# Kernel optimization log

Measured on AMD Instinct MI355X. Metric: run time of the kernel, lower is better.

Reference implementation:

```python
import jax, jax.numpy as jnp
import numpy as np

B, N, T, H = 32, 512, 3, 8
F_IN, F_HID, F_OUT = 768, 64, 64
NEG_SLOPE = 0.2
NEG_INF = -1e9


def setup_inputs() -> dict:
    key = jax.random.key(0)
    ks = jax.random.split(key, 16)
    s = 0.05
    emb = jax.random.normal(ks[0], (B, N, F_IN), jnp.float32)
    adj = jax.random.randint(ks[1], (B, N, N), 0, 2).astype(jnp.int32)
    adj = adj.at[:, jnp.arange(N), jnp.arange(N)].set(1)  # self loops so no empty rows
    vt_idx = jax.random.randint(ks[2], (B, N), 0, T)
    v_types = jax.nn.one_hot(vt_idx, T, dtype=jnp.float32)
    # layer 1 GAT params: per-type weights [T,H,f_in,f_out]
    w1 = jax.random.normal(ks[3], (T, H, F_IN, F_HID), jnp.float32) * s
    a_src1 = jax.random.normal(ks[4], (H, F_HID), jnp.float32) * s
    a_dst1 = jax.random.normal(ks[5], (H, F_HID), jnp.float32) * s
    b1 = jnp.zeros((F_HID,), jnp.float32)
    # layer 2 GAT (single head, f_in = H*F_HID)
    w2 = jax.random.normal(ks[6], (T, 1, H * F_HID, F_OUT), jnp.float32) * s
    a_src2 = jax.random.normal(ks[7], (1, F_OUT), jnp.float32) * s
    a_dst2 = jax.random.normal(ks[8], (1, F_OUT), jnp.float32) * s
    b2 = jnp.zeros((F_OUT,), jnp.float32)
    # MLP classifier: fc1 d->3d, fc2 3d->d, fc3 d->2
    fc1_w = jax.random.normal(ks[9], (F_OUT, 3 * F_OUT), jnp.float32) * s
    fc1_b = jnp.zeros((3 * F_OUT,), jnp.float32)
    fc2_w = jax.random.normal(ks[10], (3 * F_OUT, F_OUT), jnp.float32) * s
    fc2_b = jnp.zeros((F_OUT,), jnp.float32)
    fc3_w = jax.random.normal(ks[11], (F_OUT, 2), jnp.float32) * s
    fc3_b = jnp.zeros((2,), jnp.float32)
    return dict(emb=emb, adj=adj, v_types=v_types,
                w1=w1, a_src1=a_src1, a_dst1=a_dst1, b1=b1,
                w2=w2, a_src2=a_src2, a_dst2=a_dst2, b2=b2,
                fc1_w=fc1_w, fc1_b=fc1_b, fc2_w=fc2_w, fc2_b=fc2_b,
                fc3_w=fc3_w, fc3_b=fc3_b)


def _leaky_relu(x):
    return jnp.where(x >= 0, x, NEG_SLOPE * x)


def _gat(h, adj_mask, vt, w, a_src, a_dst, bias):
    # h: [B,N,f_in], vt: [B,N,T] one-hot, w: [T,Hd,f_in,f_out]
    # per-type projection then select node's type
    hpt = jnp.einsum('bni,thio->bntho', h, w)          # [B,N,T,Hd,f_out]
    hp = jnp.einsum('bnt,bntho->bnho', vt, hpt)        # [B,N,Hd,f_out]
    src = jnp.einsum('bnho,ho->bhn', hp, a_src)        # [B,Hd,N]
    dst = jnp.einsum('bnho,ho->bhn', hp, a_dst)
    e = _leaky_relu(src[:, :, :, None] + dst[:, :, None, :])  # [B,Hd,N,N]
    e = jnp.where(adj_mask[:, None, :, :], e, NEG_INF)
    attn = jax.nn.softmax(e, axis=-1)                  # attn_dropout=0.0 -> identity
    out = jnp.einsum('bhnm,bmho->bhno', attn, hp) + bias
    return out                                         # [B,Hd,N,f_out]


def reference(emb, adj, v_types, w1, a_src1, a_dst1, b1,
              w2, a_src2, a_dst2, b2,
              fc1_w, fc1_b, fc2_w, fc2_b, fc3_w, fc3_b):
    adj_mask = adj > 0
    x = _gat(emb, adj_mask, v_types, w1, a_src1, a_dst1, b1)    # [B,H,N,F_HID]
    x = jnp.transpose(x, (0, 2, 1, 3)).reshape(B, N, H * F_HID)  # concat heads
    x = jax.nn.elu(x)                                            # dropout: eval mode (identity)
    x = _gat(x, adj_mask, v_types, w2, a_src2, a_dst2, b2)       # [B,1,N,F_OUT]
    x = jax.nn.elu(x)
    x = x[:, 0, :, :]                                            # squeeze head dim -> [B,N,F_OUT]
    left = x[:, 0, :]
    right = x[:, 1, :]
    v = left * right
    v = jax.nn.relu(v @ fc1_w + fc1_b)
    v = jax.nn.relu(v @ fc2_w + fc2_b)
    scores = v @ fc3_w + fc3_b
    return jax.nn.log_softmax(scores, axis=1)
```

## Files before the change

kernel.cpp:

```cpp
#include <hip/hip_runtime.h>

#define BB   32
#define NN   512
#define NH   8
#define FIN  768
#define FHID 64
#define NROWS (BB*NN)

typedef __attribute__((ext_vector_type(8))) short bf16x8;
typedef __attribute__((ext_vector_type(4))) short s16x4;
typedef __attribute__((ext_vector_type(4))) float f32x4;
typedef unsigned long long u64;
typedef unsigned short u16;

__device__ __forceinline__ float lrelu_f(float s){ return fmaxf(s, 0.2f*s); }
__device__ __forceinline__ float elu_f(float s){ return s > 0.f ? s : expm1f(s); }
__device__ __forceinline__ short f2bf(float f){
  unsigned u = __float_as_uint(f);
  return (short)((u + 0x7fffu + ((u >> 16) & 1u)) >> 16);
}
__device__ __forceinline__ float bf2f(short s){
  return __uint_as_float(((unsigned)(u16)s) << 16);
}
__device__ __forceinline__ unsigned cvt_pk_bf16(float lo, float hi){
  unsigned r;
  asm("v_cvt_pk_bf16_f32 %0, %1, %2" : "=v"(r) : "v"(lo), "v"(hi));
  return r;
}

__global__ __launch_bounds__(256) void prep_kernel(
    const int* __restrict__ adj,
    u64* __restrict__ maskw)
{
  int row  = blockIdx.x * 4 + (threadIdx.x >> 6);
  int lane = threadIdx.x & 63;
  const int* arow = adj + (long)row * NN;
  #pragma unroll
  for (int w = 0; w < 8; ++w) {
    u64 bal = __ballot(arow[w*64 + lane] > 0);
    if (lane == 0) maskw[(long)row*8 + w] = bal;
  }
}

__global__ __launch_bounds__(256) void rowlist_kernel(
    const float* __restrict__ vt,
    int* __restrict__ rowlist, int* __restrict__ counts)
{
  __shared__ int lc[3];
  __shared__ int lbase[3];
  int tid = threadIdx.x;
  int row = blockIdx.x * 256 + tid;
  if (tid < 3) lc[tid] = 0;
  __syncthreads();
  const float* v = vt + (long)row*3;
  int t = v[1] > 0.5f ? 1 : (v[2] > 0.5f ? 2 : 0);
  int p = atomicAdd(&lc[t], 1);
  __syncthreads();
  if (tid < 3) lbase[tid] = atomicAdd(&counts[tid], lc[tid]);
  __syncthreads();
  rowlist[t*NROWS + lbase[t] + p] = row;
}

__global__ __launch_bounds__(256) void conv_w(
    const float* __restrict__ w1, const float* __restrict__ w2,
    u16* __restrict__ w1t, u16* __restrict__ w2t)
{
  __shared__ float tile[64][68];
  int bid = blockIdx.x, tid = threadIdx.x;
  const float* src; u16* dst; int K;
  if (bid < 24) { src = w1 + (long)bid*768*64; dst = w1t + (long)bid*64*768; K = 768; }
  else { int t = bid - 24; src = w2 + (long)t*512*64; dst = w2t + (long)t*64*512; K = 512; }
  int kq = blockIdx.y;
  int kstart = kq * (K >> 2), kend = kstart + (K >> 2);

  for (int k0 = kstart; k0 < kend; k0 += 64) {
    __syncthreads();
    #pragma unroll
    for (int i = 0; i < 4; ++i) {
      int kk = i*16 + (tid >> 4);
      int oo = (tid & 15) * 4;
      float4 v = *(const float4*)(src + (long)(k0 + kk)*64 + oo);
      *(float4*)&tile[kk][oo] = v;
    }
    __syncthreads();
    int o = tid >> 2, kp = (tid & 3) * 16;
    bf16x8 r0, r1;
    #pragma unroll
    for (int j = 0; j < 8; ++j) r0[j] = f2bf(tile[kp + j][o]);
    #pragma unroll
    for (int j = 0; j < 8; ++j) r1[j] = f2bf(tile[kp + 8 + j][o]);
    u16* d = dst + (long)o*K + k0 + kp;
    *(bf16x8*)d = r0;
    *(bf16x8*)(d + 8) = r1;
  }
}

__global__ __launch_bounds__(256) void gemm1_mfma(
    const float* __restrict__ emb,
    const u16* __restrict__ w1t,
    const int* __restrict__ rowlist, const int* __restrict__ counts,
    u16* __restrict__ hp1b)
{
  int i   = blockIdx.x;
  int t   = i / 352;
  int r   = i - t*352;
  int cnt = counts[t];
  int xcd = r & 7;
  int q   = r >> 3;
  int hb  = q & 3;
  int rb  = (q >> 2) * 8 + xcd;
  int r0  = rb * 64;
  if (r0 >= cnt) return;

  __shared__ short aT[2][4*66*8];
  __shared__ short bT[2][4*130*8];
  __shared__ int rowsS[64];

  int tid = threadIdx.x;
  if (tid < 64) {
    int rr = r0 + tid;
    rowsS[tid] = (rr < cnt) ? rowlist[t*NROWS + rr] : -1;
  }
  __syncthreads();

  int ar = tid >> 2, ac = tid & 3;
  int sg = rowsS[ar]; if (sg < 0) sg = rowsS[0];
  const float* aP = emb + (long)sg*768;

  int colb = tid >> 2, off = tid & 3;
  const u16* bP1 = w1t + (((long)t*8 + hb*2 + 0)*64 + colb)*768;
  const u16* bP2 = w1t + (((long)t*8 + hb*2 + 1)*64 + colb)*768;

  int wv = tid >> 6, l = tid & 63;
  int wr = wv >> 1, wc = wv & 1;
  int l15 = l & 15, lg = l >> 4;

  int aw0 = (( (ac>>1)     )*66 + ar)*8 + (ac&1)*4;
  int aw1 = (( 2 + (ac>>1) )*66 + ar)*8 + (ac&1)*4;
  int bw0 = (off*130 + colb     )*8;
  int bw1 = (off*130 + colb + 64)*8;

  f32x4 acc[2][4];
  #pragma unroll
  for (int fr = 0; fr < 2; ++fr)
    #pragma unroll
    for (int cf = 0; cf < 4; ++cf) acc[fr][cf] = (f32x4){0.f,0.f,0.f,0.f};

  float4 ra0 = *(const float4*)(aP + ac*4);
  float4 ra1 = *(const float4*)(aP + 16 + ac*4);
  bf16x8 rb1 = *(const bf16x8*)(bP1 + off*8);
  bf16x8 rb2 = *(const bf16x8*)(bP2 + off*8);
  {
    s16x4 w0, w1;
    w0[0]=f2bf(ra0.x); w0[1]=f2bf(ra0.y); w0[2]=f2bf(ra0.z); w0[3]=f2bf(ra0.w);
    w1[0]=f2bf(ra1.x); w1[1]=f2bf(ra1.y); w1[2]=f2bf(ra1.z); w1[3]=f2bf(ra1.w);
    *(s16x4*)&aT[0][aw0] = w0;
    *(s16x4*)&aT[0][aw1] = w1;
    *(bf16x8*)&bT[0][bw0] = rb1;
    *(bf16x8*)&bT[0][bw1] = rb2;
  }
  __syncthreads();

  int cur = 0;
  for (int k0 = 0; k0 < 768; k0 += 32) {
    bool more = (k0 + 32 < 768);
    if (more) {
      ra0 = *(const float4*)(aP + k0 + 32 + ac*4);
      ra1 = *(const float4*)(aP + k0 + 48 + ac*4);
      rb1 = *(const bf16x8*)(bP1 + k0 + 32 + off*8);
      rb2 = *(const bf16x8*)(bP2 + k0 + 32 + off*8);
    }
    bf16x8 af[2], bfr[4];
    #pragma unroll
    for (int fr = 0; fr < 2; ++fr)
      af[fr] = *(const bf16x8*)&aT[cur][(lg*66 + wr*32 + fr*16 + l15)*8];
    #pragma unroll
    for (int cf = 0; cf < 4; ++cf)
      bfr[cf] = *(const bf16x8*)&bT[cur][(lg*130 + wc*64 + cf*16 + l15)*8];
    #pragma unroll
    for (int fr = 0; fr < 2; ++fr)
      #pragma unroll
      for (int cf = 0; cf < 4; ++cf)
        acc[fr][cf] = __builtin_amdgcn_mfma_f32_16x16x32_bf16(af[fr], bfr[cf], acc[fr][cf], 0, 0, 0);
    if (more) {
      s16x4 w0, w1;
      w0[0]=f2bf(ra0.x); w0[1]=f2bf(ra0.y); w0[2]=f2bf(ra0.z); w0[3]=f2bf(ra0.w);
      w1[0]=f2bf(ra1.x); w1[1]=f2bf(ra1.y); w1[2]=f2bf(ra1.z); w1[3]=f2bf(ra1.w);
      *(s16x4*)&aT[cur^1][aw0] = w0;
      *(s16x4*)&aT[cur^1][aw1] = w1;
      *(bf16x8*)&bT[cur^1][bw0] = rb1;
      *(bf16x8*)&bT[cur^1][bw1] = rb2;
    }
    __syncthreads();
    cur ^= 1;
  }

  #pragma unroll
  for (int fr = 0; fr < 2; ++fr) {
    #pragma unroll
    for (int r4 = 0; r4 < 4; ++r4) {
      int rloc = wr*32 + fr*16 + lg*4 + r4;
      int rg = rowsS[rloc];
      if (rg < 0) continue;
      long obase = ((long)(rg >> 9) * 8) * 32768 + (long)(rg & 511) * 64;
      #pragma unroll
      for (int cf = 0; cf < 4; ++cf) {
        int c = wc*64 + cf*16 + l15;
        hp1b[obase + (long)(hb*2 + (c >> 6))*32768 + (c & 63)] = (u16)f2bf(acc[fr][cf][r4]);
      }
    }
  }
}

__global__ __launch_bounds__(256) void gemm2_mfma(
    const u16* __restrict__ xbf,
    const u16* __restrict__ w2t,
    const int* __restrict__ rowlist, const int* __restrict__ counts,
    float* __restrict__ hp2)
{
  int i   = blockIdx.x;
  int t   = i >> 8;
  int cnt = counts[t];
  int r0  = (i & 255) * 64;
  if (r0 >= cnt) return;

  __shared__ short aT[4*66*8];
  __shared__ short bT[4*66*8];
  __shared__ int rowsS[64];

  int tid = threadIdx.x;
  if (tid < 64) {
    int rr = r0 + tid;
    rowsS[tid] = (rr < cnt) ? rowlist[t*NROWS + rr] : -1;
  }
  __syncthreads();

  int ar = tid >> 2, ac = tid & 3;
  int sg = rowsS[ar]; if (sg < 0) sg = rowsS[0];
  long apart = ((long)(sg >> 9) * 8) * 32768 + (long)(sg & 511) * 64;

  int colb = tid >> 2, off = tid & 3;
  const u16* bP = w2t + ((long)t*64 + colb)*512;

  int wv = tid >> 6, l = tid & 63;
  int l15 = l & 15, lg = l >> 4;

  f32x4 acc[4];
  #pragma unroll
  for (int cf = 0; cf < 4; ++cf) acc[cf] = (f32x4){0.f,0.f,0.f,0.f};

  int ka0 = ac*8;
  bf16x8 ra = *(const bf16x8*)(xbf + apart + (long)(ka0 >> 6)*32768 + (ka0 & 63));
  bf16x8 rb = *(const bf16x8*)(bP + off*8);

  for (int k0 = 0; k0 < 512; k0 += 32) {
    __syncthreads();
    *(bf16x8*)&aT[(ac*66 + ar)*8]   = ra;
    *(bf16x8*)&bT[(off*66 + colb)*8] = rb;
    __syncthreads();
    if (k0 + 32 < 512) {
      int kn = k0 + 32 + ac*8;
      ra = *(const bf16x8*)(xbf + apart + (long)(kn >> 6)*32768 + (kn & 63));
      rb = *(const bf16x8*)(bP + k0 + 32 + off*8);
    }
    bf16x8 af, bfr[4];
    af = *(const bf16x8*)&aT[(lg*66 + wv*16 + l15)*8];
    #pragma unroll
    for (int cf = 0; cf < 4; ++cf)
      bfr[cf] = *(const bf16x8*)&bT[(lg*66 + cf*16 + l15)*8];
    #pragma unroll
    for (int cf = 0; cf < 4; ++cf)
      acc[cf] = __builtin_amdgcn_mfma_f32_16x16x32_bf16(af, bfr[cf], acc[cf], 0, 0, 0);
  }

  #pragma unroll
  for (int r4 = 0; r4 < 4; ++r4) {
    int rloc = wv*16 + lg*4 + r4;
    int rg = rowsS[rloc];
    if (rg < 0) continue;
    #pragma unroll
    for (int cf = 0; cf < 4; ++cf)
      hp2[(long)rg*64 + cf*16 + l15] = acc[cf][r4];
  }
}

__global__ __launch_bounds__(1024) void gat1_attn(
    u16* __restrict__ hp1b, const u64* __restrict__ maskw,
    const float* __restrict__ a_src, const float* __restrict__ a_dst,
    const float* __restrict__ b1)
{
  extern __shared__ char smc[];
  short* hpTf = (short*)smc;
  short* pSf  = (short*)(smc + 67584);
  float* srcS = (float*)(smc + 135168);
  float* dstS = (float*)(smc + 137216);
  float* asS  = (float*)(smc + 139264);
  float* adS  = (float*)(smc + 139520);
  float* rcpS = (float*)(smc + 139776);

  int bh = blockIdx.x;
  int b = bh >> 3, h = bh & 7;
  int tid = threadIdx.x;

  if (tid < 64) asS[tid] = a_src[h*64 + tid];
  else if (tid < 128) adS[tid - 64] = a_dst[h*64 + (tid - 64)];
  __syncthreads();

  {
    int m = tid >> 1, half = tid & 1;
    int koct = m >> 3, sub = m & 7;
    const u16* hpRow = hp1b + ((long)bh*NN + m)*64 + half*32;
    float ps = 0.f, pd = 0.f;
    #pragma unroll
    for (int qq = 0; qq < 4; ++qq) {
      bf16x8 hv = *(const bf16x8*)(hpRow + qq*8);
      int o0 = half*32 + qq*8;
      #pragma unroll
      for (int j = 0; j < 8; ++j) {
        float f = bf2f(hv[j]);
        ps += f * asS[o0 + j];
        pd += f * adS[o0 + j];
        hpTf[(koct*66 + o0 + j)*8 + sub] = hv[j];
      }
    }
    ps += __shfl_xor(ps, 1);
    pd += __shfl_xor(pd, 1);
    if ((tid & 1) == 0) { srcS[m] = ps; dstS[m] = pd; }
  }
  __syncthreads();

  int wv = tid >> 6, lane = tid & 63;
  int l15 = lane & 15, lg = lane >> 4;
  int cgl = wv >> 2, nt = wv & 3;
  int o_out = nt*16 + l15;
  float bb  = b1[o_out];

  float2 dst2[4];
  #pragma unroll
  for (int jj = 0; jj < 4; ++jj)
    dst2[jj] = *(const float2*)&dstS[jj*128 + 2*lane];
  int wsel = lane >> 5;
  unsigned sh = (unsigned)((2*lane) & 63);
  int pbase = ((lane >> 2)*66)*8 + 2*(lane & 3);

  for (int sup = 0; sup < 8; ++sup) {
    #pragma unroll
    for (int rr = 0; rr < 4; ++rr) {
      int rloc = wv*4 + rr;
      int row  = sup*64 + rloc;
      float srcv = srcS[row];
      const u64* mrow = maskw + ((long)(b*NN + row))*8;
      float lsum = 0.f;
      #pragma unroll
      for (int jj = 0; jj < 4; ++jj) {
        u64 w = mrow[jj*2 + wsel];
        unsigned bits = (unsigned)(w >> sh) & 3u;
        float s0 = srcv + dst2[jj].x;
        float s1 = srcv + dst2[jj].y;
        float p0 = (bits & 1u) ? __expf(lrelu_f(s0)) : 0.f;
        float p1 = (bits & 2u) ? __expf(lrelu_f(s1)) : 0.f;
        lsum += p0 + p1;
        unsigned pk = cvt_pk_bf16(p0, p1);
        *(unsigned*)&pSf[(jj*16*66)*8 + pbase + rloc*8] = pk;
      }
      #pragma unroll
      for (int mk = 1; mk <= 32; mk <<= 1) lsum += __shfl_xor(lsum, mk);
      if (lane == 0) rcpS[rloc] = 1.f / lsum;
    }
    __syncthreads();

    f32x4 acc = {0.f, 0.f, 0.f, 0.f};
    #pragma unroll
    for (int ks = 0; ks < 16; ++ks) {
      int koct = ks*4 + lg;
      bf16x8 af = *(const bf16x8*)&pSf [(koct*66 + cgl*16 + l15)*8];
      bf16x8 bf = *(const bf16x8*)&hpTf[(koct*66 + nt*16  + l15)*8];
      acc = __builtin_amdgcn_mfma_f32_16x16x32_bf16(af, bf, acc, 0, 0, 0);
    }
    #pragma unroll
    for (int reg = 0; reg < 4; ++reg) {
      int rloc = cgl*16 + lg*4 + reg;
      int row  = sup*64 + rloc;
      float v = elu_f(acc[reg] * rcpS[rloc] + bb);
      hp1b[((long)bh*NN + row)*64 + o_out] = (u16)f2bf(v);
    }
    __syncthreads();
  }
}

__global__ __launch_bounds__(256) void gat2_final(
    const float* __restrict__ hp2, const u64* __restrict__ maskw,
    const float* __restrict__ a_src2, const float* __restrict__ a_dst2,
    const float* __restrict__ b2,
    const float* __restrict__ fc1_w, const float* __restrict__ fc1_b,
    const float* __restrict__ fc2_w, const float* __restrict__ fc2_b,
    const float* __restrict__ fc3_w, const float* __restrict__ fc3_b,
    float* __restrict__ out)
{
  extern __shared__ float sm[];
  float* hpS  = sm;
  float* dstS = hpS + 32768;
  float* srcS = dstS + 512;
  float* pS   = srcS + 512;
  float* redS = pS + 512;
  float* outS = redS + 256;
  float* vS   = outS + 128;
  float* y1S  = vS + 64;
  float* redM = y1S + 192;
  float4* hpS4 = (float4*)hpS;

  int b = blockIdx.x;
  int tid = threadIdx.x;
  int og = tid & 15, m16 = tid >> 4;

  for (int it = 0; it < 32; ++it) {
    int fi = it*256 + tid;
    int m = fi >> 4, o4 = fi & 15;
    hpS4[m*16 + o4] = *(const float4*)(hp2 + (long)(b*NN + m)*64 + o4*4);
  }
  __syncthreads();

  float4 as4 = *(const float4*)(a_src2 + og*4);
  float4 ad4 = *(const float4*)(a_dst2 + og*4);
  for (int it = 0; it < 32; ++it) {
    int m = it*16 + m16;
    float4 hv = hpS4[m*16 + og];
    float ls = hv.x*as4.x + hv.y*as4.y + hv.z*as4.z + hv.w*as4.w;
    float ld = hv.x*ad4.x + hv.y*ad4.y + hv.z*ad4.z + hv.w*ad4.w;
    #pragma unroll
    for (int mk = 1; mk <= 8; mk <<= 1) {
      ls += __shfl_xor(ls, mk);
      ld += __shfl_xor(ld, mk);
    }
    if (og == 0) { srcS[m] = ls; dstS[m] = ld; }
  }
  __syncthreads();

  for (int n = 0; n < 2; ++n) {
    float srcv = srcS[n];
    const u64* mrow = maskw + (long)(b*NN + n)*8;
    int m0 = tid, m1 = tid + 256;
    u64 w0 = mrow[m0 >> 6], w1 = mrow[m1 >> 6];
    float s0 = srcv + dstS[m0], s1 = srcv + dstS[m1];
    float e0 = ((w0 >> (m0 & 63)) & 1ull) ? lrelu_f(s0) : -1.0e9f;
    float e1 = ((w1 >> (m1 & 63)) & 1ull) ? lrelu_f(s1) : -1.0e9f;
    float emax = fmaxf(e0, e1);
    #pragma unroll
    for (int mk = 1; mk <= 32; mk <<= 1) emax = fmaxf(emax, __shfl_xor(emax, mk));
    if ((tid & 63) == 0) redM[tid >> 6] = emax;
    __syncthreads();
    emax = fmaxf(fmaxf(redM[0], redM[1]), fmaxf(redM[2], redM[3]));
    float p0 = __expf(e0 - emax), p1 = __expf(e1 - emax);
    pS[m0] = p0; pS[m1] = p1;
    float lsum = p0 + p1;
    #pragma unroll
    for (int mk = 1; mk <= 32; mk <<= 1) lsum += __shfl_xor(lsum, mk);
    if ((tid & 63) == 0) redM[4 + (tid >> 6)] = lsum;
    __syncthreads();
    float rcp = 1.f / (redM[4] + redM[5] + redM[6] + redM[7]);

    float4 acc = make_float4(0.f,0.f,0.f,0.f);
    for (int mm = 0; mm < 32; ++mm) {
      int m = mm*16 + m16;
      float4 hv = hpS4[m*16 + og];
      float p = pS[m];
      acc.x += hv.x*p; acc.y += hv.y*p; acc.z += hv.z*p; acc.w += hv.w*p;
    }
    acc.x += __shfl_xor(acc.x, 16); acc.y += __shfl_xor(acc.y, 16);
    acc.z += __shfl_xor(acc.z, 16); acc.w += __shfl_xor(acc.w, 16);
    acc.x += __shfl_xor(acc.x, 32); acc.y += __shfl_xor(acc.y, 32);
    acc.z += __shfl_xor(acc.z, 32); acc.w += __shfl_xor(acc.w, 32);
    __syncthreads();
    if ((tid & 63) < 16) ((float4*)redS)[(tid >> 6)*16 + (tid & 15)] = acc;
    __syncthreads();
    if (tid < 16) {
      float4 s = make_float4(0.f,0.f,0.f,0.f);
      #pragma unroll
      for (int w = 0; w < 4; ++w) {
        float4 v = ((float4*)redS)[w*16 + tid];
        s.x += v.x; s.y += v.y; s.z += v.z; s.w += v.w;
      }
      float4 bv = *(const float4*)(b2 + tid*4);
      outS[n*64 + tid*4 + 0] = elu_f(s.x*rcp + bv.x);
      outS[n*64 + tid*4 + 1] = elu_f(s.y*rcp + bv.y);
      outS[n*64 + tid*4 + 2] = elu_f(s.z*rcp + bv.z);
      outS[n*64 + tid*4 + 3] = elu_f(s.w*rcp + bv.w);
    }
    __syncthreads();
  }

  if (tid < 64) vS[tid] = outS[tid] * outS[64 + tid];
  __syncthreads();
  if (tid < 192) {
    float a = fc1_b[tid];
    for (int o = 0; o < 64; ++o) a += vS[o]*fc1_w[o*192 + tid];
    y1S[tid] = a > 0.f ? a : 0.f;
  }
  __syncthreads();
  if (tid < 64) {
    float a = fc2_b[tid];
    for (int j = 0; j < 192; ++j) a += y1S[j]*fc2_w[j*64 + tid];
    vS[tid] = a > 0.f ? a : 0.f;
  }
  __syncthreads();
  if (tid == 0) {
    float t0 = fc3_b[0], t1 = fc3_b[1];
    for (int k = 0; k < 64; ++k) {
      float y = vS[k];
      t0 += y*fc3_w[k*2 + 0];
      t1 += y*fc3_w[k*2 + 1];
    }
    float mx = fmaxf(t0, t1);
    float lse = mx + logf(__expf(t0 - mx) + __expf(t1 - mx));
    out[b*2 + 0] = t0 - lse;
    out[b*2 + 1] = t1 - lse;
  }
}

extern "C" void kernel_launch(void* const* d_in, const int* in_sizes, int n_in,
                              void* d_out, int out_size, void* d_ws, size_t ws_size,
                              hipStream_t stream) {
  const float* emb    = (const float*)d_in[0];
  const int*   adj    = (const int*)d_in[1];
  const float* vt     = (const float*)d_in[2];
  const float* w1     = (const float*)d_in[3];
  const float* a_src1 = (const float*)d_in[4];
  const float* a_dst1 = (const float*)d_in[5];
  const float* b1     = (const float*)d_in[6];
  const float* w2     = (const float*)d_in[7];
  const float* a_src2 = (const float*)d_in[8];
  const float* a_dst2 = (const float*)d_in[9];
  const float* b2     = (const float*)d_in[10];
  const float* fc1_w  = (const float*)d_in[11];
  const float* fc1_b  = (const float*)d_in[12];
  const float* fc2_w  = (const float*)d_in[13];
  const float* fc2_b  = (const float*)d_in[14];
  const float* fc3_w  = (const float*)d_in[15];
  const float* fc3_b  = (const float*)d_in[16];

  char* ws = (char*)d_ws;
  int* counts  = (int*)ws;
  int* rowlist = (int*)(ws + 4096);
  u64* maskw   = (u64*)(ws + 204800);
  u16* w1t     = (u16*)(ws + 1310720);
  u16* w2t     = (u16*)(ws + 3670016);
  u16* hp1b    = (u16*)(ws + 3932160);
  float* hp2   = (float*)(ws + 20709376);

  hipMemsetAsync(counts, 0, 16, stream);
  prep_kernel<<<NROWS/4, 256, 0, stream>>>(adj, maskw);
  rowlist_kernel<<<NROWS/256, 256, 0, stream>>>(vt, rowlist, counts);
  conv_w<<<dim3(27, 4), 256, 0, stream>>>(w1, w2, w1t, w2t);

  gemm1_mfma<<<dim3(1056), 256, 0, stream>>>(emb, w1t, rowlist, counts, hp1b);

  size_t sm1 = 140032;
  gat1_attn<<<BB*NH, 1024, sm1, stream>>>(hp1b, maskw, a_src1, a_dst1, b1);

  gemm2_mfma<<<dim3(768), 256, 0, stream>>>(hp1b, w2t, rowlist, counts, hp2);

  size_t sm2 = (size_t)(32768 + 512 + 512 + 512 + 256 + 128 + 64 + 192 + 8) * 4;
  gat2_final<<<BB, 256, sm2, stream>>>(hp2, maskw, a_src2, a_dst2, b2,
                                       fc1_w, fc1_b, fc2_w, fc2_b, fc3_w, fc3_b,
                                       (float*)d_out);
}
```

Measured before the change: 147.1 us.

## Use FP8 MFMA for GAT1 attention and split each head across two blocks

Switches the layer-1 attention aggregation from bf16 to fp8 operands: the attention probabilities and the transposed projected features are stored as fp8 in LDS and multiplied with the 16x16x32 fp8 MFMA. This halves LDS use, so each (batch, head) can be split over two blocks that each handle half of the row super-tiles, doubling grid size from 256 to 512 blocks. Output now goes to a separate buffer, because the two blocks of a head both read the full hp1b input. The cost is much lower precision (e4m3) in the attention-weighted sum, which risks accuracy, and the src/dst score and LDS transpose setup is done twice per head.

```diff
diff --git a/kernel.cpp b/kernel.cpp
--- a/kernel.cpp
+++ b/kernel.cpp
@@ -12,6 +12,7 @@
 typedef __attribute__((ext_vector_type(4))) float f32x4;
 typedef unsigned long long u64;
 typedef unsigned short u16;
+typedef long i64;
 
 __device__ __forceinline__ float lrelu_f(float s){ return fmaxf(s, 0.2f*s); }
 __device__ __forceinline__ float elu_f(float s){ return s > 0.f ? s : expm1f(s); }
@@ -22,10 +23,8 @@
 __device__ __forceinline__ float bf2f(short s){
   return __uint_as_float(((unsigned)(u16)s) << 16);
 }
-__device__ __forceinline__ unsigned cvt_pk_bf16(float lo, float hi){
-  unsigned r;
-  asm("v_cvt_pk_bf16_f32 %0, %1, %2" : "=v"(r) : "v"(lo), "v"(hi));
-  return r;
+__device__ __forceinline__ unsigned cvt_pk_fp8(float lo, float hi){
+  return (unsigned)__builtin_amdgcn_cvt_pk_fp8_f32(lo, hi, 0, false);
 }
 
 __global__ __launch_bounds__(256) void prep_kernel(
@@ -285,20 +284,21 @@
 }
 
 __global__ __launch_bounds__(1024) void gat1_attn(
-    u16* __restrict__ hp1b, const u64* __restrict__ maskw,
+    const u16* __restrict__ hp1b, const u64* __restrict__ maskw,
     const float* __restrict__ a_src, const float* __restrict__ a_dst,
-    const float* __restrict__ b1)
+    const float* __restrict__ b1, u16* __restrict__ xbf)
 {
   extern __shared__ char smc[];
-  short* hpTf = (short*)smc;
-  short* pSf  = (short*)(smc + 67584);
-  float* srcS = (float*)(smc + 135168);
-  float* dstS = (float*)(smc + 137216);
-  float* asS  = (float*)(smc + 139264);
-  float* adS  = (float*)(smc + 139520);
-  float* rcpS = (float*)(smc + 139776);
-
-  int bh = blockIdx.x;
+  char*  hpTf = smc;
+  char*  pSf  = smc + 33792;
+  float* srcS = (float*)(smc + 67584);
+  float* dstS = (float*)(smc + 69632);
+  float* asS  = (float*)(smc + 71680);
+  float* adS  = (float*)(smc + 71936);
+  float* rcpS = (float*)(smc + 72192);
+
+  int bid = blockIdx.x;
+  int bh = bid >> 1, qh = bid & 1;
   int b = bh >> 3, h = bh & 7;
   int tid = threadIdx.x;
 
@@ -308,7 +308,7 @@
 
   {
     int m = tid >> 1, half = tid & 1;
-    int koct = m >> 3, sub = m & 7;
+    int koct = m >> 3, kin = m & 7;
     const u16* hpRow = hp1b + ((long)bh*NN + m)*64 + half*32;
     float ps = 0.f, pd = 0.f;
     #pragma unroll
@@ -320,7 +320,7 @@
         float f = bf2f(hv[j]);
         ps += f * asS[o0 + j];
         pd += f * adS[o0 + j];
-        hpTf[(koct*66 + o0 + j)*8 + sub] = hv[j];
+        hpTf[(koct*66 + o0 + j)*8 + kin] = (char)(cvt_pk_fp8(f, f) & 0xffu);
       }
     }
     ps += __shfl_xor(ps, 1);
@@ -343,7 +343,8 @@
   unsigned sh = (unsigned)((2*lane) & 63);
   int pbase = ((lane >> 2)*66)*8 + 2*(lane & 3);
 
-  for (int sup = 0; sup < 8; ++sup) {
+  for (int s = 0; s < 4; ++s) {
+    int sup = qh*4 + s;
     #pragma unroll
     for (int rr = 0; rr < 4; ++rr) {
       int rloc = wv*4 + rr;
@@ -360,8 +361,7 @@
         float p0 = (bits & 1u) ? __expf(lrelu_f(s0)) : 0.f;
         float p1 = (bits & 2u) ? __expf(lrelu_f(s1)) : 0.f;
         lsum += p0 + p1;
-        unsigned pk = cvt_pk_bf16(p0, p1);
-        *(unsigned*)&pSf[(jj*16*66)*8 + pbase + rloc*8] = pk;
+        *(u16*)&pSf[(jj*16*66)*8 + pbase + rloc*8] = (u16)cvt_pk_fp8(p0, p1);
       }
       #pragma unroll
       for (int mk = 1; mk <= 32; mk <<= 1) lsum += __shfl_xor(lsum, mk);
@@ -373,16 +373,16 @@
     #pragma unroll
     for (int ks = 0; ks < 16; ++ks) {
       int koct = ks*4 + lg;
-      bf16x8 af = *(const bf16x8*)&pSf [(koct*66 + cgl*16 + l15)*8];
-      bf16x8 bf = *(const bf16x8*)&hpTf[(koct*66 + nt*16  + l15)*8];
-      acc = __builtin_amdgcn_mfma_f32_16x16x32_bf16(af, bf, acc, 0, 0, 0);
+      i64 af = *(const i64*)&pSf [(koct*66 + cgl*16 + l15)*8];
+      i64 bf = *(const i64*)&hpTf[(koct*66 + nt*16  + l15)*8];
+      acc = __builtin_amdgcn_mfma_f32_16x16x32_fp8_fp8(af, bf, acc, 0, 0, 0);
     }
     #pragma unroll
     for (int reg = 0; reg < 4; ++reg) {
       int rloc = cgl*16 + lg*4 + reg;
       int row  = sup*64 + rloc;
       float v = elu_f(acc[reg] * rcpS[rloc] + bb);
-      hp1b[((long)bh*NN + row)*64 + o_out] = (u16)f2bf(v);
+      xbf[((long)bh*NN + row)*64 + o_out] = (u16)f2bf(v);
     }
     __syncthreads();
   }
@@ -546,6 +546,7 @@
   u16* w2t     = (u16*)(ws + 3670016);
   u16* hp1b    = (u16*)(ws + 3932160);
   float* hp2   = (float*)(ws + 20709376);
+  u16* xbf     = (u16*)(ws + 24903680);
 
   hipMemsetAsync(counts, 0, 16, stream);
   prep_kernel<<<NROWS/4, 256, 0, stream>>>(adj, maskw);
@@ -554,10 +555,10 @@
 
   gemm1_mfma<<<dim3(1056), 256, 0, stream>>>(emb, w1t, rowlist, counts, hp1b);
 
-  size_t sm1 = 140032;
-  gat1_attn<<<BB*NH, 1024, sm1, stream>>>(hp1b, maskw, a_src1, a_dst1, b1);
-
-  gemm2_mfma<<<dim3(768), 256, 0, stream>>>(hp1b, w2t, rowlist, counts, hp2);
+  size_t sm1 = 72448;
+  gat1_attn<<<BB*NH*2, 1024, sm1, stream>>>(hp1b, maskw, a_src1, a_dst1, b1, xbf);
+
+  gemm2_mfma<<<dim3(768), 256, 0, stream>>>(xbf, w2t, rowlist, counts, hp2);
 
   size_t sm2 = (size_t)(32768 + 512 + 512 + 512 + 256 + 128 + 64 + 192 + 8) * 4;
   gat2_final<<<BB, 256, sm2, stream>>>(hp2, maskw, a_src2, a_dst2, b2,
```

New measurement: 147.9 us. About the same (+0.5%).
